# Performance work log

Hardware: AMD Instinct MI355X
Metric: run time of the kernel (lower is better)

The kernel has to match this reference:

```python
import jax, jax.numpy as jnp
import numpy as np


def setup_inputs() -> dict:
    key = jax.random.key(0)
    ks = jax.random.split(key, 7)
    bs, win_len, num_obj, d = 4, 64, 36, 2048
    s = 1.0 / np.sqrt(d)
    return {
        "region_feats": jax.random.normal(ks[0], (bs, win_len, num_obj, d), jnp.float32),
        "Wq": jax.random.normal(ks[1], (d, d), jnp.float32) * s,
        "bq": jax.random.normal(ks[2], (d,), jnp.float32) * 0.01,
        "Wk": jax.random.normal(ks[3], (d, d), jnp.float32) * s,
        "bk": jax.random.normal(ks[4], (d,), jnp.float32) * 0.01,
        "Wu": jax.random.normal(ks[5], (d, 1024), jnp.float32) * s,
        "bu": jax.random.normal(ks[6], (1024,), jnp.float32) * 0.01,
    }


def reference(region_feats, Wq, bq, Wk, bk, Wu, bu):
    bs, win_len, num_obj, d = region_feats.shape
    feats = region_feats.reshape(bs, win_len * num_obj, d)  # [b, n, d]
    q = feats @ Wq + bq                                     # [b, n, d]
    k = feats @ Wk + bk                                     # [b, n, d]
    adj = jnp.einsum('bnd,bmd->bnm', q, k)                  # unscaled QK^T, [b, n, n]
    adj_norm = jax.nn.softmax(adj, axis=-1)
    v = feats @ Wu + bu                                     # [b, n, 1024]
    out = jnp.einsum('bnm,bmv->bnv', adj_norm, v)
    return out.reshape(bs, win_len, num_obj, -1)
```

## Files before the change

### kernel.cpp

```cpp
#include <hip/hip_runtime.h>


typedef unsigned short u16;
typedef unsigned int   u32;
typedef signed char    i8;
typedef _Float16 f16;
typedef f16    f16x8 __attribute__((ext_vector_type(8)));
typedef float  f32x4 __attribute__((ext_vector_type(4)));
typedef int    i32x4 __attribute__((ext_vector_type(4)));
typedef u32    u32x4 __attribute__((ext_vector_type(4)));
typedef u16    u16x4 __attribute__((ext_vector_type(4)));

#define WAIT_VM8   0x0F78
#define WAIT_VM4   0x0F74
#define WAIT_VM0   0x0F70
#define WAIT_LGKM0 0xC07F

__device__ __forceinline__ void gload16(const void* g, void* l) {
    __builtin_amdgcn_global_load_lds(
        (const __attribute__((address_space(1))) unsigned int*)g,
        (__attribute__((address_space(3))) unsigned int*)l, 16, 0, 0);
}

__device__ __forceinline__ void tile_swizzle(int& tx, int& ty) {
    const int gx = gridDim.x, gy = gridDim.y;
    const int lin = blockIdx.y * gx + blockIdx.x;
    const int G = 4;
    const int gid = lin / (G * gx);
    const int g0 = gid * G;
    const int gh = min(G, gy - g0);
    const int rem = lin - gid * (G * gx);
    ty = g0 + rem % gh;
    tx = rem / gh;
}

__device__ __forceinline__ void digits256(float v, float s, i8& d1, i8& d0) {
    float f = fminf(fmaxf(v * s, -32600.0f), 32600.0f);
    int r = __float2int_rn(f);
    int a1 = (r + 128) >> 8;
    int a0 = r - (a1 << 8);
    d1 = (i8)a1;
    d0 = (i8)a0;
}

template <int EPI>
__device__ __forceinline__ void gemm_i8_body(
    i8* ldsb, int tx, int ty, int z,
    const i8* __restrict__ Ah, const i8* __restrict__ Al,
    const i8* __restrict__ Bh, const i8* __restrict__ Bl,
    i8* __restrict__ Qh, i8* __restrict__ Ql, float* __restrict__ Cf,
    float oscale, int N, int K, long strA, long strB, long strC) {
    const int tid  = threadIdx.x;
    const int lane = tid & 63;
    const int wv   = tid >> 6;
    const int wm   = wv >> 1, wn = wv & 1;
    const int l16  = lane & 15, kq = lane >> 4;
    const long rowBase = (long)ty * 128;
    const long colBase = (long)tx * 128;

    const i8* pAh = Ah + (long)z * strA;
    const i8* pAl = Al + (long)z * strA;
    const i8* pBh = Bh + (long)z * strB;
    const i8* pBl = Bl + (long)z * strB;

    const int l4r = lane >> 2, l4c = lane & 3;
    int rin[2];
    u32 voffA[2], voffB[2];
    int ldsoff[2];
    #pragma unroll
    for (int h = 0; h < 2; ++h) {
        rin[h] = h * 64 + wv * 16 + l4r;
        const int kw = (l4c - (rin[h] >> 1)) & 3;
        voffA[h] = (u32)((rowBase + rin[h]) * (long)K) + kw * 16;
        voffB[h] = (u32)((colBase + rin[h]) * (long)K) + kw * 16;
        ldsoff[h] = (h * 64 + wv * 16) * 64;
    }

    int aoff[4], boff[4];
    #pragma unroll
    for (int i = 0; i < 4; ++i) {
        const int rA = wm * 64 + i * 16 + l16;
        aoff[i] = rA * 64 + ((kq + (rA >> 1)) & 3) * 16;
        const int rB = wn * 64 + i * 16 + l16;
        boff[i] = rB * 64 + ((kq + (rB >> 1)) & 3) * 16;
    }

    const i32x4 izero = {0, 0, 0, 0};
    i32x4 ahh[4][4], acx[4][4], all_[4][4];
    #pragma unroll
    for (int i = 0; i < 4; ++i)
        #pragma unroll
        for (int j = 0; j < 4; ++j) { ahh[i][j] = izero; acx[i][j] = izero; all_[i][j] = izero; }

    const int nk = K >> 6;

    #pragma unroll
    for (int h = 0; h < 2; ++h) {
        gload16(pAh + voffA[h], ldsb         + ldsoff[h]);
        gload16(pAl + voffA[h], ldsb + 8192  + ldsoff[h]);
        gload16(pBh + voffB[h], ldsb + 16384 + ldsoff[h]);
        gload16(pBl + voffB[h], ldsb + 24576 + ldsoff[h]);
    }

    for (int kt = 0; kt < nk; ++kt) {
        const int cur = kt & 1;
        if (kt + 1 < nk) {
            const long ko = (long)(kt + 1) * 64;
            i8* nb = ldsb + (1 - cur) * 32768;
            #pragma unroll
            for (int h = 0; h < 2; ++h) {
                gload16(pAh + voffA[h] + ko, nb         + ldsoff[h]);
                gload16(pAl + voffA[h] + ko, nb + 8192  + ldsoff[h]);
                gload16(pBh + voffB[h] + ko, nb + 16384 + ldsoff[h]);
                gload16(pBl + voffB[h] + ko, nb + 24576 + ldsoff[h]);
            }
            __builtin_amdgcn_s_waitcnt(WAIT_VM8);
        } else {
            __builtin_amdgcn_s_waitcnt(WAIT_VM0);
        }
        __builtin_amdgcn_s_barrier();

        const i8* base = ldsb + cur * 32768;
        i32x4 fbh[4], fbl[4];
        #pragma unroll
        for (int j = 0; j < 4; ++j) {
            fbh[j] = *(const i32x4*)(base + 16384 + boff[j]);
            fbl[j] = *(const i32x4*)(base + 24576 + boff[j]);
        }
        #pragma unroll
        for (int i = 0; i < 4; ++i) {
            i32x4 fah = *(const i32x4*)(base + aoff[i]);
            i32x4 fal = *(const i32x4*)(base + 8192 + aoff[i]);
            #pragma unroll
            for (int j = 0; j < 4; ++j) {
                ahh[i][j]  = __builtin_amdgcn_mfma_i32_16x16x64_i8(fah, fbh[j], ahh[i][j], 0, 0, 0);
                acx[i][j]  = __builtin_amdgcn_mfma_i32_16x16x64_i8(fah, fbl[j], acx[i][j], 0, 0, 0);
                acx[i][j]  = __builtin_amdgcn_mfma_i32_16x16x64_i8(fal, fbh[j], acx[i][j], 0, 0, 0);
                all_[i][j] = __builtin_amdgcn_mfma_i32_16x16x64_i8(fal, fbl[j], all_[i][j], 0, 0, 0);
            }
        }
        __builtin_amdgcn_s_waitcnt(WAIT_LGKM0);
        __builtin_amdgcn_s_barrier();
    }

    #pragma unroll
    for (int i = 0; i < 4; ++i) {
        const long gr0 = rowBase + wm * 64 + i * 16 + kq * 4;
        #pragma unroll
        for (int j = 0; j < 4; ++j) {
            const long gc = colBase + wn * 64 + j * 16 + l16;
            #pragma unroll
            for (int r = 0; r < 4; ++r) {
                const float comb = 65536.0f * (float)ahh[i][j][r] +
                                     256.0f * (float)acx[i][j][r] +
                                             (float)all_[i][j][r];
                const long o = (gr0 + r) * (long)N + gc;
                if constexpr (EPI == 0) {
                    i8 d1, d0;
                    digits256(comb, oscale, d1, d0);
                    Qh[o] = d1;
                    Ql[o] = d0;
                } else {
                    Cf[(long)z * strC + o] = comb * oscale;
                }
            }
        }
    }
}

template <int EPI>
__device__ __forceinline__ void gemm_f16_body(
    i8* ldsb, int tx, int ty, int z,
    const u16* __restrict__ A, const u16* __restrict__ B,
    u16* __restrict__ Ch, float* __restrict__ Cf,
    const float* __restrict__ bias,
    int N, int K, long strA, long strB, long strC) {
    const int tid  = threadIdx.x;
    const int lane = tid & 63;
    const int wv   = tid >> 6;
    const int wm   = wv >> 1, wn = wv & 1;
    const int l16  = lane & 15, kq = lane >> 4;
    const long rowBase = (long)ty * 128;
    const long colBase = (long)tx * 128;

    const u16* pA = A + (long)z * strA;
    const u16* pB = B + (long)z * strB;

    const int l4r = lane >> 2, l4c = lane & 3;
    u32 voffA[2], voffB[2];
    int ldsoff[2];
    #pragma unroll
    for (int h = 0; h < 2; ++h) {
        const int rin = h * 64 + wv * 16 + l4r;
        const int kw = (l4c - (rin >> 1)) & 3;
        voffA[h] = (u32)((rowBase + rin) * (long)K) + kw * 8;
        voffB[h] = (u32)((colBase + rin) * (long)K) + kw * 8;
        ldsoff[h] = (h * 64 + wv * 16) * 64;
    }
    int aoff[4], boff[4];
    #pragma unroll
    for (int i = 0; i < 4; ++i) {
        const int rA = wm * 64 + i * 16 + l16;
        aoff[i] = rA * 64 + ((kq + (rA >> 1)) & 3) * 16;
        const int rB = wn * 64 + i * 16 + l16;
        boff[i] = rB * 64 + ((kq + (rB >> 1)) & 3) * 16;
    }

    const f32x4 vzero = {0.f, 0.f, 0.f, 0.f};
    f32x4 acc[4][4];
    #pragma unroll
    for (int i = 0; i < 4; ++i)
        #pragma unroll
        for (int j = 0; j < 4; ++j) acc[i][j] = vzero;

    const int nk = K >> 5;

    #pragma unroll
    for (int h = 0; h < 2; ++h) {
        gload16(pA + voffA[h], ldsb        + ldsoff[h]);
        gload16(pB + voffB[h], ldsb + 8192 + ldsoff[h]);
    }

    for (int kt = 0; kt < nk; ++kt) {
        const int cur = kt & 1;
        if (kt + 1 < nk) {
            const long ko = (long)(kt + 1) * 32;
            i8* nb = ldsb + (1 - cur) * 16384;
            #pragma unroll
            for (int h = 0; h < 2; ++h) {
                gload16(pA + voffA[h] + ko, nb        + ldsoff[h]);
                gload16(pB + voffB[h] + ko, nb + 8192 + ldsoff[h]);
            }
            __builtin_amdgcn_s_waitcnt(WAIT_VM4);
        } else {
            __builtin_amdgcn_s_waitcnt(WAIT_VM0);
        }
        __builtin_amdgcn_s_barrier();

        const i8* base = ldsb + cur * 16384;
        f16x8 fa[4];
        #pragma unroll
        for (int i = 0; i < 4; ++i)
            fa[i] = __builtin_bit_cast(f16x8, *(const u32x4*)(base + aoff[i]));
        #pragma unroll
        for (int j = 0; j < 4; ++j) {
            f16x8 fb = __builtin_bit_cast(f16x8, *(const u32x4*)(base + 8192 + boff[j]));
            #pragma unroll
            for (int i = 0; i < 4; ++i)
                acc[i][j] = __builtin_amdgcn_mfma_f32_16x16x32_f16(fa[i], fb, acc[i][j], 0, 0, 0);
        }
        __builtin_amdgcn_s_waitcnt(WAIT_LGKM0);
        __builtin_amdgcn_s_barrier();
    }

    #pragma unroll
    for (int i = 0; i < 4; ++i) {
        const long gr0 = rowBase + wm * 64 + i * 16 + kq * 4;
        #pragma unroll
        for (int j = 0; j < 4; ++j) {
            const long gc = colBase + wn * 64 + j * 16 + l16;
            f32x4 a = acc[i][j];
            if constexpr (EPI == 2) {
                const int b  = (int)(gr0 / 2304);
                const int n0 = (int)(gr0 - (long)b * 2304);
                u16x4 o4;
                #pragma unroll
                for (int r = 0; r < 4; ++r) o4[r] = __builtin_bit_cast(u16, (f16)a[r]);
                *(u16x4*)&Ch[(long)b * (1024L * 2304) + gc * 2304 + n0] = o4;
            } else {
                float* C = Cf + (long)z * strC;
                const float bv = bias[gc];
                #pragma unroll
                for (int r = 0; r < 4; ++r) C[(gr0 + r) * (long)N + gc] = a[r] + bv;
            }
        }
    }
}

__device__ __forceinline__ void quantFc_body(long row, float* red,
                                             const float* __restrict__ F,
                                             const float* __restrict__ u,
                                             u16* __restrict__ F16,
                                             i8* __restrict__ hi,
                                             i8* __restrict__ lo,
                                             float* __restrict__ c) {
    const int tid = threadIdx.x;
    const float* fr = F + row * 2048;
    float dot = 0.f;
    #pragma unroll
    for (int t = 0; t < 8; ++t) {
        const int i = t * 256 + tid;
        const float v = fr[i];
        F16[row * 2048 + i] = __builtin_bit_cast(u16, (f16)v);
        i8 d1, d0;
        digits256(v, 5440.0f, d1, d0);
        hi[row * 2048 + i] = d1;
        lo[row * 2048 + i] = d0;
        dot += v * u[i];
    }
    #pragma unroll
    for (int off = 32; off >= 1; off >>= 1) dot += __shfl_down(dot, off);
    if ((tid & 63) == 0) red[tid >> 6] = dot;
    __syncthreads();
    if (tid == 0) c[row] = red[0] + red[1] + red[2] + red[3];
}

__global__ __launch_bounds__(256) void prep_k(const float* __restrict__ Wk,
                                              const float* __restrict__ bq,
                                              float* __restrict__ u,
                                              const float* __restrict__ Wq,
                                              i8* __restrict__ Wqh, i8* __restrict__ Wql,
                                              i8* __restrict__ Wkh, i8* __restrict__ Wkl,
                                              const float* __restrict__ Wu,
                                              u16* __restrict__ WuT) {
    __shared__ __align__(16) float sm[32 * 33];
    const int tid = threadIdx.x;
    const int id = blockIdx.x;
    if (id < 2048) {
        const float* ar = Wk + (long)id * 2048;
        float s = 0.f;
        #pragma unroll
        for (int t = 0; t < 8; ++t) s += ar[t * 256 + tid] * bq[t * 256 + tid];
        #pragma unroll
        for (int off = 32; off >= 1; off >>= 1) s += __shfl_down(s, off);
        if ((tid & 63) == 0) sm[tid >> 6] = s;
        __syncthreads();
        if (tid == 0) u[id] = sm[0] + sm[1] + sm[2] + sm[3];
    } else if (id < 4096) {
        const int w  = id - 2048;
        const int bx = (w & 31) * 32;
        const int by = (w >> 5) * 32;
        const int lx = tid & 31, ly = tid >> 5;
        float (*t)[33] = (float (*)[33])sm;
        #pragma unroll
        for (int dy = 0; dy < 32; dy += 8)
            t[ly + dy][lx] = Wu[(long)(by + ly + dy) * 1024 + bx + lx];
        __syncthreads();
        #pragma unroll
        for (int dy = 0; dy < 32; dy += 8)
            WuT[(long)(bx + ly + dy) * 2048 + by + lx] =
                __builtin_bit_cast(u16, (f16)t[lx][ly + dy]);
    } else {
        long j = (long)id - 4096;
        const float* src;
        i8 *dh, *dl;
        if (j < 16384) { src = Wq; dh = Wqh; dl = Wql; }
        else           { j -= 16384; src = Wk; dh = Wkh; dl = Wkl; }
        const long i = j * 256 + tid;
        i8 d1, d0;
        digits256(src[i], 261120.0f, d1, d0);
        dh[i] = d1;
        dl[i] = d0;
    }
}

__global__ __launch_bounds__(256, 2) void fused_qfc_mt(
    const float* __restrict__ F, const float* __restrict__ u,
    u16* __restrict__ F16, i8* __restrict__ Fh, i8* __restrict__ Fl,
    float* __restrict__ c,
    const i8* __restrict__ Wqh, const i8* __restrict__ Wql,
    const i8* __restrict__ Wkh, const i8* __restrict__ Wkl,
    i8* __restrict__ Mth, i8* __restrict__ Mtl) {
    __shared__ __align__(16) i8 lds[2][32768];
    const int b = blockIdx.x;
    if (b < 256) {
        gemm_i8_body<0>(&lds[0][0], b & 15, b >> 4, 0,
                        Wkh, Wkl, Wqh, Wql, Mth, Mtl, nullptr,
                        3.8296569e-06f, 2048, 2048, 0L, 0L, 0L);
    } else {
        quantFc_body((long)b - 256, (float*)&lds[0][0], F, u, F16, Fh, Fl, c);
    }
}

__global__ __launch_bounds__(256, 2) void fused_sv(
    const i8* __restrict__ Fh, const i8* __restrict__ Fl,
    const i8* __restrict__ Mth, const i8* __restrict__ Mtl,
    i8* __restrict__ Sh, i8* __restrict__ Sl,
    const u16* __restrict__ F16, const u16* __restrict__ WuT,
    u16* __restrict__ vT) {
    __shared__ __align__(16) i8 lds[2][32768];
    const int bx = blockIdx.x, by = blockIdx.y;
    if (bx < 16) {
        gemm_i8_body<0>(&lds[0][0], bx, by, 0,
                        Fh, Fl, Mth, Mtl, Sh, Sl, nullptr,
                        3.8296569e-06f, 2048, 2048, 0L, 0L, 0L);
    } else {
        gemm_f16_body<2>(&lds[0][0], bx - 16, by, 0,
                         F16, WuT, vT, nullptr, nullptr,
                         1024, 2048, 0L, 0L, 0L);
    }
}

template <int EPI>
__global__ __launch_bounds__(256, 2) void gemm_i8_k(
    const i8* __restrict__ Ah, const i8* __restrict__ Al,
    const i8* __restrict__ Bh, const i8* __restrict__ Bl,
    i8* __restrict__ Qh, i8* __restrict__ Ql, float* __restrict__ Cf,
    float oscale, int N, int K, long strA, long strB, long strC) {
    __shared__ __align__(16) i8 lds[2][32768];
    int tx, ty;
    tile_swizzle(tx, ty);
    gemm_i8_body<EPI>(&lds[0][0], tx, ty, blockIdx.z,
                      Ah, Al, Bh, Bl, Qh, Ql, Cf, oscale, N, K, strA, strB, strC);
}

template <int EPI>
__global__ __launch_bounds__(256, 3) void gemm_f16_k(
    const u16* __restrict__ A, const u16* __restrict__ B,
    u16* __restrict__ Ch, float* __restrict__ Cf,
    const float* __restrict__ bias,
    int N, int K, long strA, long strB, long strC) {
    __shared__ __align__(16) i8 lds[2][16384];
    int tx, ty;
    tile_swizzle(tx, ty);
    gemm_f16_body<EPI>(&lds[0][0], tx, ty, blockIdx.z,
                       A, B, Ch, Cf, bias, N, K, strA, strB, strC);
}

__global__ __launch_bounds__(256) void softmax_k(const float* __restrict__ adj,
                                                 const float* __restrict__ c,
                                                 u16* __restrict__ P) {
    const int n = 2304;
    const int row = blockIdx.x, b = blockIdx.y;
    const int tid = threadIdx.x;
    const float* ar = adj + ((long)b * n + row) * (long)n;
    const float* cb = c + (long)b * n;
    u16* pr = P + ((long)b * n + row) * (long)n;

    float v[9];
    float mx = -3.0e38f;
    #pragma unroll
    for (int t = 0; t < 9; ++t) {
        const int i = t * 256 + tid;
        const float x = ar[i] + cb[i];
        v[t] = x;
        mx = fmaxf(mx, x);
    }
    #pragma unroll
    for (int off = 32; off >= 1; off >>= 1) mx = fmaxf(mx, __shfl_down(mx, off));
    __shared__ float red[4];
    if ((tid & 63) == 0) red[tid >> 6] = mx;
    __syncthreads();
    mx = fmaxf(fmaxf(red[0], red[1]), fmaxf(red[2], red[3]));

    float s = 0.f;
    #pragma unroll
    for (int t = 0; t < 9; ++t) {
        const float e = __expf(v[t] - mx);
        v[t] = e;
        s += e;
    }
    #pragma unroll
    for (int off = 32; off >= 1; off >>= 1) s += __shfl_down(s, off);
    __shared__ float red2[4];
    if ((tid & 63) == 0) red2[tid >> 6] = s;
    __syncthreads();
    s = red2[0] + red2[1] + red2[2] + red2[3];
    const float inv = 1.0f / s;
    #pragma unroll
    for (int t = 0; t < 9; ++t)
        pr[t * 256 + tid] = __builtin_bit_cast(u16, (f16)(v[t] * inv));
}

extern "C" void kernel_launch(void* const* d_in, const int* in_sizes, int n_in,
                              void* d_out, int out_size, void* d_ws, size_t ws_size,
                              hipStream_t stream) {
    (void)in_sizes; (void)n_in; (void)out_size; (void)ws_size;
    const float* F  = (const float*)d_in[0];
    const float* Wq = (const float*)d_in[1];
    const float* bq = (const float*)d_in[2];
    const float* Wk = (const float*)d_in[3];
    const float* Wu = (const float*)d_in[5];
    const float* bu = (const float*)d_in[6];
    float* out = (float*)d_out;

    char* ws = (char*)d_ws;
    const long o_F16  = 0L;
    const long o_Fh8  = 37748736L;
    const long o_Fl8  = 56623104L;
    const long o_Sh8  = 75497472L;
    const long o_Sl8  = 94371840L;
    const long o_adj  = 113246208L;
    const long o_P    = 198180864L;
    const long o_vT   = 240648192L;
    const long o_WuT  = 259522560L;
    const long o_Wqh  = 263716864L;
    const long o_Wql  = 267911168L;
    const long o_Wkh  = 272105472L;
    const long o_Wkl  = 276299776L;
    const long o_Mth  = 280494080L;
    const long o_Mtl  = 284688384L;
    const long o_u    = 288882688L;
    const long o_c    = 288890880L;

    u16* F16 = (u16*)(ws + o_F16);
    i8*  Fh8 = (i8*)(ws + o_Fh8);   i8* Fl8 = (i8*)(ws + o_Fl8);
    i8*  Sh8 = (i8*)(ws + o_Sh8);   i8* Sl8 = (i8*)(ws + o_Sl8);
    float* adj = (float*)(ws + o_adj);
    u16* P   = (u16*)(ws + o_P);
    u16* vT  = (u16*)(ws + o_vT);
    u16* WuT = (u16*)(ws + o_WuT);
    i8*  Wqh = (i8*)(ws + o_Wqh);   i8* Wql = (i8*)(ws + o_Wql);
    i8*  Wkh = (i8*)(ws + o_Wkh);   i8* Wkl = (i8*)(ws + o_Wkl);
    i8*  Mth = (i8*)(ws + o_Mth);   i8* Mtl = (i8*)(ws + o_Mtl);
    float* u = (float*)(ws + o_u);
    float* c = (float*)(ws + o_c);

    prep_k<<<36864, 256, 0, stream>>>(Wk, bq, u, Wq, Wqh, Wql, Wkh, Wkl, Wu, WuT);

    fused_qfc_mt<<<9472, 256, 0, stream>>>(F, u, F16, Fh8, Fl8, c,
                                           Wqh, Wql, Wkh, Wkl, Mth, Mtl);

    fused_sv<<<dim3(24, 72, 1), 256, 0, stream>>>(Fh8, Fl8, Mth, Mtl, Sh8, Sl8,
                                                  F16, WuT, vT);

    gemm_i8_k<1><<<dim3(18, 18, 4), 256, 0, stream>>>(
        Sh8, Sl8, Fh8, Fl8, nullptr, nullptr, adj,
        3.3791083e-08f, 2304, 2048,
        2304L * 2048, 2304L * 2048, 2304L * 2304);

    softmax_k<<<dim3(2304, 4, 1), 256, 0, stream>>>(adj, c, P);

    gemm_f16_k<3><<<dim3(8, 18, 4), 256, 0, stream>>>(
        P, vT, nullptr, out, bu, 1024, 2304,
        2304L * 2304, 1024L * 2304, 2304L * 1024);
}
```

Before: 632.3 us.

## Use 8 waves per block in GEMM kernels with 2x4 warp tiling

Doubles the block size from 256 to 512 threads for the GEMM and fused kernels, rearranging waves into a 2x4 grid so each wave computes a 64x32 sub-tile instead of 64x64. Each thread now issues half as many global-to-LDS loads per k-step, and the waitcnt thresholds are lowered to match. The row-prep helper in fused_qfc_mt is adjusted for 512 threads, reducing 8 partial sums. The aim is to lower per-thread accumulator register pressure and raise wave-level parallelism for hiding latency, at the cost of more waves sharing LDS bandwidth and barriers.

```diff
diff --git a/kernel.cpp b/kernel.cpp
--- a/kernel.cpp
+++ b/kernel.cpp
@@ -11,8 +11,8 @@
 typedef u32    u32x4 __attribute__((ext_vector_type(4)));
 typedef u16    u16x4 __attribute__((ext_vector_type(4)));
 
-#define WAIT_VM8   0x0F78
 #define WAIT_VM4   0x0F74
+#define WAIT_VM2   0x0F72
 #define WAIT_VM0   0x0F70
 #define WAIT_LGKM0 0xC07F
 
@@ -53,7 +53,7 @@
     const int tid  = threadIdx.x;
     const int lane = tid & 63;
     const int wv   = tid >> 6;
-    const int wm   = wv >> 1, wn = wv & 1;
+    const int wm   = wv >> 2, wn = wv & 3;
     const int l16  = lane & 15, kq = lane >> 4;
     const long rowBase = (long)ty * 128;
     const long colBase = (long)tx * 128;
@@ -64,66 +64,57 @@
     const i8* pBl = Bl + (long)z * strB;
 
     const int l4r = lane >> 2, l4c = lane & 3;
-    int rin[2];
-    u32 voffA[2], voffB[2];
-    int ldsoff[2];
-    #pragma unroll
-    for (int h = 0; h < 2; ++h) {
-        rin[h] = h * 64 + wv * 16 + l4r;
-        const int kw = (l4c - (rin[h] >> 1)) & 3;
-        voffA[h] = (u32)((rowBase + rin[h]) * (long)K) + kw * 16;
-        voffB[h] = (u32)((colBase + rin[h]) * (long)K) + kw * 16;
-        ldsoff[h] = (h * 64 + wv * 16) * 64;
-    }
-
-    int aoff[4], boff[4];
+    const int rin = wv * 16 + l4r;
+    const int kw  = (l4c - (rin >> 1)) & 3;
+    const u32 voffA = (u32)((rowBase + rin) * (long)K) + kw * 16;
+    const u32 voffB = (u32)((colBase + rin) * (long)K) + kw * 16;
+    const int ldsoff = wv * 16 * 64;
+
+    int aoff[4], boff[2];
     #pragma unroll
     for (int i = 0; i < 4; ++i) {
         const int rA = wm * 64 + i * 16 + l16;
         aoff[i] = rA * 64 + ((kq + (rA >> 1)) & 3) * 16;
-        const int rB = wn * 64 + i * 16 + l16;
-        boff[i] = rB * 64 + ((kq + (rB >> 1)) & 3) * 16;
+    }
+    #pragma unroll
+    for (int j = 0; j < 2; ++j) {
+        const int rB = wn * 32 + j * 16 + l16;
+        boff[j] = rB * 64 + ((kq + (rB >> 1)) & 3) * 16;
     }
 
     const i32x4 izero = {0, 0, 0, 0};
-    i32x4 ahh[4][4], acx[4][4], all_[4][4];
+    i32x4 ahh[4][2], acx[4][2], all_[4][2];
     #pragma unroll
     for (int i = 0; i < 4; ++i)
         #pragma unroll
-        for (int j = 0; j < 4; ++j) { ahh[i][j] = izero; acx[i][j] = izero; all_[i][j] = izero; }
+        for (int j = 0; j < 2; ++j) { ahh[i][j] = izero; acx[i][j] = izero; all_[i][j] = izero; }
 
     const int nk = K >> 6;
 
-    #pragma unroll
-    for (int h = 0; h < 2; ++h) {
-        gload16(pAh + voffA[h], ldsb         + ldsoff[h]);
-        gload16(pAl + voffA[h], ldsb + 8192  + ldsoff[h]);
-        gload16(pBh + voffB[h], ldsb + 16384 + ldsoff[h]);
-        gload16(pBl + voffB[h], ldsb + 24576 + ldsoff[h]);
-    }
+    gload16(pAh + voffA, ldsb         + ldsoff);
+    gload16(pAl + voffA, ldsb + 8192  + ldsoff);
+    gload16(pBh + voffB, ldsb + 16384 + ldsoff);
+    gload16(pBl + voffB, ldsb + 24576 + ldsoff);
 
     for (int kt = 0; kt < nk; ++kt) {
         const int cur = kt & 1;
         if (kt + 1 < nk) {
             const long ko = (long)(kt + 1) * 64;
             i8* nb = ldsb + (1 - cur) * 32768;
-            #pragma unroll
-            for (int h = 0; h < 2; ++h) {
-                gload16(pAh + voffA[h] + ko, nb         + ldsoff[h]);
-                gload16(pAl + voffA[h] + ko, nb + 8192  + ldsoff[h]);
-                gload16(pBh + voffB[h] + ko, nb + 16384 + ldsoff[h]);
-                gload16(pBl + voffB[h] + ko, nb + 24576 + ldsoff[h]);
-            }
-            __builtin_amdgcn_s_waitcnt(WAIT_VM8);
+            gload16(pAh + voffA + ko, nb         + ldsoff);
+            gload16(pAl + voffA + ko, nb + 8192  + ldsoff);
+            gload16(pBh + voffB + ko, nb + 16384 + ldsoff);
+            gload16(pBl + voffB + ko, nb + 24576 + ldsoff);
+            __builtin_amdgcn_s_waitcnt(WAIT_VM4);
         } else {
             __builtin_amdgcn_s_waitcnt(WAIT_VM0);
         }
         __builtin_amdgcn_s_barrier();
 
         const i8* base = ldsb + cur * 32768;
-        i32x4 fbh[4], fbl[4];
-        #pragma unroll
-        for (int j = 0; j < 4; ++j) {
+        i32x4 fbh[2], fbl[2];
+        #pragma unroll
+        for (int j = 0; j < 2; ++j) {
             fbh[j] = *(const i32x4*)(base + 16384 + boff[j]);
             fbl[j] = *(const i32x4*)(base + 24576 + boff[j]);
         }
@@ -132,7 +123,7 @@
             i32x4 fah = *(const i32x4*)(base + aoff[i]);
             i32x4 fal = *(const i32x4*)(base + 8192 + aoff[i]);
             #pragma unroll
-            for (int j = 0; j < 4; ++j) {
+            for (int j = 0; j < 2; ++j) {
                 ahh[i][j]  = __builtin_amdgcn_mfma_i32_16x16x64_i8(fah, fbh[j], ahh[i][j], 0, 0, 0);
                 acx[i][j]  = __builtin_amdgcn_mfma_i32_16x16x64_i8(fah, fbl[j], acx[i][j], 0, 0, 0);
                 acx[i][j]  = __builtin_amdgcn_mfma_i32_16x16x64_i8(fal, fbh[j], acx[i][j], 0, 0, 0);
@@ -147,8 +138,8 @@
     for (int i = 0; i < 4; ++i) {
         const long gr0 = rowBase + wm * 64 + i * 16 + kq * 4;
         #pragma unroll
-        for (int j = 0; j < 4; ++j) {
-            const long gc = colBase + wn * 64 + j * 16 + l16;
+        for (int j = 0; j < 2; ++j) {
+            const long gc = colBase + wn * 32 + j * 16 + l16;
             #pragma unroll
             for (int r = 0; r < 4; ++r) {
                 const float comb = 65536.0f * (float)ahh[i][j][r] +
@@ -178,7 +169,7 @@
     const int tid  = threadIdx.x;
     const int lane = tid & 63;
     const int wv   = tid >> 6;
-    const int wm   = wv >> 1, wn = wv & 1;
+    const int wm   = wv >> 2, wn = wv & 3;
     const int l16  = lane & 15, kq = lane >> 4;
     const long rowBase = (long)ty * 128;
     const long colBase = (long)tx * 128;
@@ -187,51 +178,44 @@
     const u16* pB = B + (long)z * strB;
 
     const int l4r = lane >> 2, l4c = lane & 3;
-    u32 voffA[2], voffB[2];
-    int ldsoff[2];
-    #pragma unroll
-    for (int h = 0; h < 2; ++h) {
-        const int rin = h * 64 + wv * 16 + l4r;
-        const int kw = (l4c - (rin >> 1)) & 3;
-        voffA[h] = (u32)((rowBase + rin) * (long)K) + kw * 8;
-        voffB[h] = (u32)((colBase + rin) * (long)K) + kw * 8;
-        ldsoff[h] = (h * 64 + wv * 16) * 64;
-    }
-    int aoff[4], boff[4];
+    const int rin = wv * 16 + l4r;
+    const int kw  = (l4c - (rin >> 1)) & 3;
+    const u32 voffA = (u32)((rowBase + rin) * (long)K) + kw * 8;
+    const u32 voffB = (u32)((colBase + rin) * (long)K) + kw * 8;
+    const int ldsoff = wv * 16 * 64;
+
+    int aoff[4], boff[2];
     #pragma unroll
     for (int i = 0; i < 4; ++i) {
         const int rA = wm * 64 + i * 16 + l16;
         aoff[i] = rA * 64 + ((kq + (rA >> 1)) & 3) * 16;
-        const int rB = wn * 64 + i * 16 + l16;
-        boff[i] = rB * 64 + ((kq + (rB >> 1)) & 3) * 16;
+    }
+    #pragma unroll
+    for (int j = 0; j < 2; ++j) {
+        const int rB = wn * 32 + j * 16 + l16;
+        boff[j] = rB * 64 + ((kq + (rB >> 1)) & 3) * 16;
     }
 
     const f32x4 vzero = {0.f, 0.f, 0.f, 0.f};
-    f32x4 acc[4][4];
+    f32x4 acc[4][2];
     #pragma unroll
     for (int i = 0; i < 4; ++i)
         #pragma unroll
-        for (int j = 0; j < 4; ++j) acc[i][j] = vzero;
+        for (int j = 0; j < 2; ++j) acc[i][j] = vzero;
 
     const int nk = K >> 5;
 
-    #pragma unroll
-    for (int h = 0; h < 2; ++h) {
-        gload16(pA + voffA[h], ldsb        + ldsoff[h]);
-        gload16(pB + voffB[h], ldsb + 8192 + ldsoff[h]);
-    }
+    gload16(pA + voffA, ldsb        + ldsoff);
+    gload16(pB + voffB, ldsb + 8192 + ldsoff);
 
     for (int kt = 0; kt < nk; ++kt) {
         const int cur = kt & 1;
         if (kt + 1 < nk) {
             const long ko = (long)(kt + 1) * 32;
             i8* nb = ldsb + (1 - cur) * 16384;
-            #pragma unroll
-            for (int h = 0; h < 2; ++h) {
-                gload16(pA + voffA[h] + ko, nb        + ldsoff[h]);
-                gload16(pB + voffB[h] + ko, nb + 8192 + ldsoff[h]);
-            }
-            __builtin_amdgcn_s_waitcnt(WAIT_VM4);
+            gload16(pA + voffA + ko, nb        + ldsoff);
+            gload16(pB + voffB + ko, nb + 8192 + ldsoff);
+            __builtin_amdgcn_s_waitcnt(WAIT_VM2);
         } else {
             __builtin_amdgcn_s_waitcnt(WAIT_VM0);
         }
@@ -243,7 +227,7 @@
         for (int i = 0; i < 4; ++i)
             fa[i] = __builtin_bit_cast(f16x8, *(const u32x4*)(base + aoff[i]));
         #pragma unroll
-        for (int j = 0; j < 4; ++j) {
+        for (int j = 0; j < 2; ++j) {
             f16x8 fb = __builtin_bit_cast(f16x8, *(const u32x4*)(base + 8192 + boff[j]));
             #pragma unroll
             for (int i = 0; i < 4; ++i)
@@ -257,8 +241,8 @@
     for (int i = 0; i < 4; ++i) {
         const long gr0 = rowBase + wm * 64 + i * 16 + kq * 4;
         #pragma unroll
-        for (int j = 0; j < 4; ++j) {
-            const long gc = colBase + wn * 64 + j * 16 + l16;
+        for (int j = 0; j < 2; ++j) {
+            const long gc = colBase + wn * 32 + j * 16 + l16;
             f32x4 a = acc[i][j];
             if constexpr (EPI == 2) {
                 const int b  = (int)(gr0 / 2304);
@@ -288,8 +272,8 @@
     const float* fr = F + row * 2048;
     float dot = 0.f;
     #pragma unroll
-    for (int t = 0; t < 8; ++t) {
-        const int i = t * 256 + tid;
+    for (int t = 0; t < 4; ++t) {
+        const int i = t * 512 + tid;
         const float v = fr[i];
         F16[row * 2048 + i] = __builtin_bit_cast(u16, (f16)v);
         i8 d1, d0;
@@ -302,7 +286,12 @@
     for (int off = 32; off >= 1; off >>= 1) dot += __shfl_down(dot, off);
     if ((tid & 63) == 0) red[tid >> 6] = dot;
     __syncthreads();
-    if (tid == 0) c[row] = red[0] + red[1] + red[2] + red[3];
+    if (tid == 0) {
+        float s = 0.f;
+        #pragma unroll
+        for (int w = 0; w < 8; ++w) s += red[w];
+        c[row] = s;
+    }
 }
 
 __global__ __launch_bounds__(256) void prep_k(const float* __restrict__ Wk,
@@ -354,7 +343,7 @@
     }
 }
 
-__global__ __launch_bounds__(256, 2) void fused_qfc_mt(
+__global__ __launch_bounds__(512, 2) void fused_qfc_mt(
     const float* __restrict__ F, const float* __restrict__ u,
     u16* __restrict__ F16, i8* __restrict__ Fh, i8* __restrict__ Fl,
     float* __restrict__ c,
@@ -372,7 +361,7 @@
     }
 }
 
-__global__ __launch_bounds__(256, 2) void fused_sv(
+__global__ __launch_bounds__(512, 2) void fused_sv(
     const i8* __restrict__ Fh, const i8* __restrict__ Fl,
     const i8* __restrict__ Mth, const i8* __restrict__ Mtl,
     i8* __restrict__ Sh, i8* __restrict__ Sl,
@@ -392,7 +381,7 @@
 }
 
 template <int EPI>
-__global__ __launch_bounds__(256, 2) void gemm_i8_k(
+__global__ __launch_bounds__(512, 2) void gemm_i8_k(
     const i8* __restrict__ Ah, const i8* __restrict__ Al,
     const i8* __restrict__ Bh, const i8* __restrict__ Bl,
     i8* __restrict__ Qh, i8* __restrict__ Ql, float* __restrict__ Cf,
@@ -405,7 +394,7 @@
 }
 
 template <int EPI>
-__global__ __launch_bounds__(256, 3) void gemm_f16_k(
+__global__ __launch_bounds__(512, 2) void gemm_f16_k(
     const u16* __restrict__ A, const u16* __restrict__ B,
     u16* __restrict__ Ch, float* __restrict__ Cf,
     const float* __restrict__ bias,
@@ -508,20 +497,20 @@
 
     prep_k<<<36864, 256, 0, stream>>>(Wk, bq, u, Wq, Wqh, Wql, Wkh, Wkl, Wu, WuT);
 
-    fused_qfc_mt<<<9472, 256, 0, stream>>>(F, u, F16, Fh8, Fl8, c,
+    fused_qfc_mt<<<9472, 512, 0, stream>>>(F, u, F16, Fh8, Fl8, c,
                                            Wqh, Wql, Wkh, Wkl, Mth, Mtl);
 
-    fused_sv<<<dim3(24, 72, 1), 256, 0, stream>>>(Fh8, Fl8, Mth, Mtl, Sh8, Sl8,
+    fused_sv<<<dim3(24, 72, 1), 512, 0, stream>>>(Fh8, Fl8, Mth, Mtl, Sh8, Sl8,
                                                   F16, WuT, vT);
 
-    gemm_i8_k<1><<<dim3(18, 18, 4), 256, 0, stream>>>(
+    gemm_i8_k<1><<<dim3(18, 18, 4), 512, 0, stream>>>(
         Sh8, Sl8, Fh8, Fl8, nullptr, nullptr, adj,
         3.3791083e-08f, 2304, 2048,
         2304L * 2048, 2304L * 2048, 2304L * 2304);
 
     softmax_k<<<dim3(2304, 4, 1), 256, 0, stream>>>(adj, c, P);
 
-    gemm_f16_k<3><<<dim3(8, 18, 4), 256, 0, stream>>>(
+    gemm_f16_k<3><<<dim3(8, 18, 4), 512, 0, stream>>>(
         P, vT, nullptr, out, bu, 1024, 2304,
         2304L * 2304, 1024L * 2304, 2304L * 1024);
 }
```

Measured after the change: 664.9 us. 1.05x slower.
